# Kernel tuning notes

Measured on AMD Instinct MI355X. Metric: run time of the kernel, lower is better.

The kernel has to match this reference:

```python
import jax, jax.numpy as jnp
import numpy as np

B, T, D = 1, 8192, 1024
H, DH = 16, 64
WIN = 128          # attention window (tokens on each side)
WB = 128
NB = T // WB
EPS = 1e-5


def _layernorm(x, g, b):
    mu = jnp.mean(x, axis=-1, keepdims=True)
    var = jnp.mean(jnp.square(x - mu), axis=-1, keepdims=True)
    return (x - mu) * jax.lax.rsqrt(var + EPS) * g + b


def _band_mask():
    # query offset i in [0, WB), key offset j in [0, 3*WB) within [prev|self|next] blocks
    i = jnp.arange(WB)[:, None]
    j = jnp.arange(3 * WB)[None, :]
    rel = j - WB - i                      # key_pos - query_pos
    band = jnp.abs(rel) <= WIN            # sliding window |i-j| <= W (matches torch mask)
    blk = jnp.arange(NB)[:, None, None]
    key_pos = blk * WB + (j - WB)[None]   # absolute key position
    return band[None] & (key_pos >= 0) & (key_pos < T)   # [NB, WB, 3*WB]


def _local_attention(q, k, v):
    # q,k,v: [B,H,T,DH] -> block-local SDPA, mathematically identical to
    # full SDPA with the additive band mask in the torch code.
    def blocks(t):
        return t.reshape(B, H, NB, WB, DH)
    qb = blocks(q)
    kp = jnp.pad(blocks(k), ((0, 0), (0, 0), (1, 1), (0, 0), (0, 0)))
    vp = jnp.pad(blocks(v), ((0, 0), (0, 0), (1, 1), (0, 0), (0, 0)))
    # gather [prev, self, next] key/value blocks: [B,H,NB,3*WB,DH]
    k3 = jnp.concatenate([kp[:, :, s:s + NB] for s in range(3)], axis=3)
    v3 = jnp.concatenate([vp[:, :, s:s + NB] for s in range(3)], axis=3)
    scores = jnp.einsum('bhnqd,bhnkd->bhnqk', qb, k3) / np.sqrt(DH).astype(np.float32)
    mask = _band_mask()                                   # [NB,WB,3WB]
    scores = jnp.where(mask[None, None], scores, -jnp.inf)
    attn = jax.nn.softmax(scores, axis=-1)
    out = jnp.einsum('bhnqk,bhnkd->bhnqd', attn, v3)      # [B,H,NB,WB,DH]
    return out.reshape(B, H, T, DH)


def setup_inputs() -> dict:
    key = jax.random.key(0)
    ks = jax.random.split(key, 7)
    s = 0.02
    return {
        'x': jax.random.normal(ks[0], (B, T, D), jnp.float32),
        'wq': jax.random.normal(ks[1], (D, D), jnp.float32) * s,
        'wk': jax.random.normal(ks[2], (D, D), jnp.float32) * s,
        'wv': jax.random.normal(ks[3], (D, D), jnp.float32) * s,
        'wo': jax.random.normal(ks[4], (D, D), jnp.float32) * s,
        'wg': jax.random.normal(ks[5], (D, 2 * D), jnp.float32) * s,
        'wd': jax.random.normal(ks[6], (2 * D, D), jnp.float32) * s,
        'norm_g': jnp.ones((D,), jnp.float32),
        'norm_b': jnp.zeros((D,), jnp.float32),
        'ffn_g': jnp.ones((D,), jnp.float32),
        'ffn_b': jnp.zeros((D,), jnp.float32),
    }


def reference(x, wq, wk, wv, wo, wg, wd, norm_g, norm_b, ffn_g, ffn_b):
    h = _layernorm(x, norm_g, norm_b)
    def heads(t):  # [B,T,D] -> [B,H,T,DH]
        return t.reshape(B, T, H, DH).transpose(0, 2, 1, 3)
    q, k, v = heads(h @ wq), heads(h @ wk), heads(h @ wv)
    attn_out = _local_attention(q, k, v)                     # [B,H,T,DH]
    attn_out = attn_out.transpose(0, 2, 1, 3).reshape(B, T, D)
    x = x + attn_out @ wo
    h = _layernorm(x, ffn_g, ffn_b)
    x = x + jax.nn.silu(h @ wg) @ wd
    return x
```

## Files before the change

kernel.cpp:

```cpp
#include <hip/hip_runtime.h>
#include <cstdint>

#define T_DIM 8192
#define D_DIM 1024
#define NB_DIM 64
#define QKS 2048

typedef __bf16 bf16x8 __attribute__((ext_vector_type(8)));
typedef __bf16 bf16x4 __attribute__((ext_vector_type(4)));
typedef float f32x4 __attribute__((ext_vector_type(4)));

#define MFMA16(a, b, c) __builtin_amdgcn_mfma_f32_16x16x32_bf16((a), (b), (c), 0, 0, 0)
#define BAR() asm volatile("s_barrier" ::: "memory")
#define VMCNT(n) asm volatile("s_waitcnt vmcnt(" #n ")" ::: "memory")

__device__ __forceinline__ void gld_lds16(const void* gsrc, void* ldst) {
  __builtin_amdgcn_global_load_lds(
      (__attribute__((address_space(1))) void*)(uintptr_t)gsrc,
      (__attribute__((address_space(3))) void*)(uintptr_t)ldst,
      16, 0, 0);
}

__global__ __launch_bounds__(256) void transpose_all(
    const float* __restrict__ wq, const float* __restrict__ wk,
    const float* __restrict__ wv, const float* __restrict__ wo,
    const float* __restrict__ wg, const float* __restrict__ wd,
    __bf16* __restrict__ wqkT, __bf16* __restrict__ wvT,
    __bf16* __restrict__ woT, __bf16* __restrict__ wgT,
    __bf16* __restrict__ wdT) {
  __shared__ float tile[32][33];
  const int bid = (int)blockIdx.x;
  const float* W; __bf16* Wt; int K, N, n0, k0, local;
  if (bid < 1024)      { W = wq; Wt = wqkT;            K = 1024; N = 1024; local = bid; }
  else if (bid < 2048) { W = wk; Wt = wqkT + 1048576;  K = 1024; N = 1024; local = bid - 1024; }
  else if (bid < 3072) { W = wv; Wt = wvT;             K = 1024; N = 1024; local = bid - 2048; }
  else if (bid < 4096) { W = wo; Wt = woT;             K = 1024; N = 1024; local = bid - 3072; }
  else if (bid < 6144) { W = wg; Wt = wgT;             K = 1024; N = 2048; local = bid - 4096; }
  else                 { W = wd; Wt = wdT;             K = 2048; N = 1024; local = bid - 6144; }
  if (N == 2048) { n0 = (local & 63) * 32; k0 = (local >> 6) * 32; }
  else           { n0 = (local & 31) * 32; k0 = (local >> 5) * 32; }
  const int tx = threadIdx.x & 31, ty = threadIdx.x >> 5;
#pragma unroll
  for (int i = 0; i < 32; i += 8)
    tile[ty + i][tx] = W[(size_t)(k0 + ty + i) * N + n0 + tx];
  __syncthreads();
#pragma unroll
  for (int i = 0; i < 32; i += 8)
    Wt[(size_t)(n0 + ty + i) * K + k0 + tx] = (__bf16)tile[tx][ty + i];
}

template <typename TI>
__global__ __launch_bounds__(256) void ln_kernel(
    const TI* __restrict__ x, const float* __restrict__ g,
    const float* __restrict__ b, __bf16* __restrict__ out) {
  __shared__ float red[8];
  const int row = blockIdx.x, tid = threadIdx.x;
  float v0, v1, v2, v3;
  if constexpr (sizeof(TI) == 4) {
    const float4 v = ((const float4*)(x + (size_t)row * D_DIM))[tid];
    v0 = v.x; v1 = v.y; v2 = v.z; v3 = v.w;
  } else {
    const bf16x4 v = ((const bf16x4*)(x + (size_t)row * D_DIM))[tid];
    v0 = (float)v[0]; v1 = (float)v[1]; v2 = (float)v[2]; v3 = (float)v[3];
  }
  float s = v0 + v1 + v2 + v3;
#pragma unroll
  for (int off = 32; off >= 1; off >>= 1) s += __shfl_xor(s, off, 64);
  if ((tid & 63) == 0) red[tid >> 6] = s;
  __syncthreads();
  const float mean = (red[0] + red[1] + red[2] + red[3]) * (1.0f / D_DIM);
  const float d0 = v0 - mean, d1 = v1 - mean, d2 = v2 - mean, d3 = v3 - mean;
  float ss = d0 * d0 + d1 * d1 + d2 * d2 + d3 * d3;
#pragma unroll
  for (int off = 32; off >= 1; off >>= 1) ss += __shfl_xor(ss, off, 64);
  if ((tid & 63) == 0) red[4 + (tid >> 6)] = ss;
  __syncthreads();
  const float var = (red[4] + red[5] + red[6] + red[7]) * (1.0f / D_DIM);
  const float rstd = rsqrtf(var + 1e-5f);
  const float4 gg = ((const float4*)g)[tid];
  const float4 bb = ((const float4*)b)[tid];
  bf16x4 o;
  o[0] = (__bf16)(d0 * rstd * gg.x + bb.x);
  o[1] = (__bf16)(d1 * rstd * gg.y + bb.y);
  o[2] = (__bf16)(d2 * rstd * gg.z + bb.z);
  o[3] = (__bf16)(d3 * rstd * gg.w + bb.w);
  *(bf16x4*)(out + (size_t)row * D_DIM + tid * 4) = o;
}

template <int BM_, int EPI>
__global__ __launch_bounds__(512, 2) void gemm8(
    const __bf16* __restrict__ A, const __bf16* __restrict__ Bt,
    const void* __restrict__ Res, void* __restrict__ Cout,
    int M, int N, int K, int nbn) {
  constexpr int MF = BM_ / 32;
  constexpr int MH = MF / 2;
  constexpr int SA = 8 * MF;
  constexpr int LA = BM_ / 128;
  constexpr int ATILE = BM_ * 64;
  constexpr int AHALF = BM_ * 32;
  constexpr int BOFF = 2 * ATILE;
  __shared__ __bf16 lds[2 * BM_ * 64 + 32768];

  const int tid = threadIdx.x;
  const int l = tid & 63, w = tid >> 6;
  const int lr = l & 15, lg = l >> 4;
  const int wr = w >> 2, wc = w & 3;
  const int nwg = gridDim.x;
  const int bid = (int)blockIdx.x;
  const int swz = (bid & 7) * (nwg >> 3) + (bid >> 3);
  const int bm = swz / nbn, bn = swz % nbn;
  const int am0 = bm * BM_, bn0 = bn * 256;

  f32x4 acc[MF][4];
  const f32x4 z4 = {0.f, 0.f, 0.f, 0.f};
#pragma unroll
  for (int m = 0; m < MF; ++m)
#pragma unroll
    for (int n = 0; n < 4; ++n) acc[m][n] = z4;

  auto stageA = [&](int h, int b, int k0) {
#pragma unroll
    for (int r = 0; r < LA; ++r) {
      const int ci = r * 512 + tid;
      const int wri = ci >> 3, c8 = ci & 7;
      const int ra = (wri % SA) + (wri / SA) * (2 * SA) + h * SA;
      gld_lds16(A + (size_t)(am0 + ra) * K + k0 + ((c8 ^ (wri & 7)) << 3),
                (__bf16*)lds + b * ATILE + h * AHALF + ci * 8);
    }
  };
  auto stageB = [&](int h, int b, int k0) {
#pragma unroll
    for (int r = 0; r < 2; ++r) {
      const int ci = r * 512 + tid;
      const int wri = ci >> 3, c8 = ci & 7;
      const int rb = (wri & 31) + (wri >> 5) * 64 + h * 32;
      gld_lds16(Bt + (size_t)(bn0 + rb) * K + k0 + ((c8 ^ (wri & 7)) << 3),
                (__bf16*)lds + BOFF + b * 16384 + h * 8192 + ci * 8);
    }
  };

  const int x7 = lr & 7;
  const int aoff0 = (lr + wr * SA) * 64 + ((lg) ^ x7) * 8;
  const int aoff1 = (lr + wr * SA) * 64 + ((4 + lg) ^ x7) * 8;
  const int boff0 = BOFF + (lr + wc * 32) * 64 + ((lg) ^ x7) * 8;
  const int boff1 = BOFF + (lr + wc * 32) * 64 + ((4 + lg) ^ x7) * 8;

  const int nt = K >> 6;
  stageA(0, 0, 0);
  stageB(1, 0, 0);
  stageB(0, 0, 0);
  stageA(1, 0, 0);
  stageA(0, 1, 64);
  stageB(1, 1, 64);
  if constexpr (BM_ == 256) VMCNT(6); else VMCNT(4);
  BAR();

  int buf = 0;
  bf16x8 afr[MH][2], bfr0[2][2], bfr1[2][2];
  for (int t = 0; t < nt; ++t) {
    const bool s1 = (t + 1 < nt);
    const bool s2 = (t + 2 < nt);
    const int nb = buf ^ 1;
    const int k1 = (t + 1) << 6;
    const int k2 = (t + 2) << 6;
    const __bf16* pa0 = lds + buf * ATILE + aoff0;
    const __bf16* pa1 = lds + buf * ATILE + aoff1;
    const __bf16* pb0 = lds + buf * 16384 + boff0;
    const __bf16* pb1 = lds + buf * 16384 + boff1;

#pragma unroll
    for (int i = 0; i < MH; ++i) {
      afr[i][0] = *(const bf16x8*)(pa0 + i * 1024);
      afr[i][1] = *(const bf16x8*)(pa1 + i * 1024);
    }
#pragma unroll
    for (int j = 0; j < 2; ++j) {
      bfr0[j][0] = *(const bf16x8*)(pb0 + j * 1024);
      bfr0[j][1] = *(const bf16x8*)(pb1 + j * 1024);
    }
    if (s1) stageB(0, nb, k1);
    BAR();
    __builtin_amdgcn_s_setprio(1);
#pragma unroll
    for (int kk = 0; kk < 2; ++kk)
#pragma unroll
      for (int i = 0; i < MH; ++i)
#pragma unroll
        for (int j = 0; j < 2; ++j)
          acc[i][j] = MFMA16(afr[i][kk], bfr0[j][kk], acc[i][j]);
    __builtin_amdgcn_s_setprio(0);

#pragma unroll
    for (int j = 0; j < 2; ++j) {
      bfr1[j][0] = *(const bf16x8*)(pb0 + 8192 + j * 1024);
      bfr1[j][1] = *(const bf16x8*)(pb1 + 8192 + j * 1024);
    }
    if (s1) {
      stageA(1, nb, k1);
      if constexpr (BM_ == 256) VMCNT(8); else VMCNT(6);
    } else {
      VMCNT(0);
    }
    BAR();
    __builtin_amdgcn_s_setprio(1);
#pragma unroll
    for (int kk = 0; kk < 2; ++kk)
#pragma unroll
      for (int i = 0; i < MH; ++i)
#pragma unroll
        for (int j = 0; j < 2; ++j)
          acc[i][2 + j] = MFMA16(afr[i][kk], bfr1[j][kk], acc[i][2 + j]);
    __builtin_amdgcn_s_setprio(0);

#pragma unroll
    for (int i = 0; i < MH; ++i) {
      afr[i][0] = *(const bf16x8*)(pa0 + AHALF + i * 1024);
      afr[i][1] = *(const bf16x8*)(pa1 + AHALF + i * 1024);
    }
    if (s2) stageA(0, buf, k2);
    BAR();
    __builtin_amdgcn_s_setprio(1);
#pragma unroll
    for (int kk = 0; kk < 2; ++kk)
#pragma unroll
      for (int i = 0; i < MH; ++i)
#pragma unroll
        for (int j = 0; j < 2; ++j)
          acc[MH + i][2 + j] = MFMA16(afr[i][kk], bfr1[j][kk], acc[MH + i][2 + j]);
    __builtin_amdgcn_s_setprio(0);

    if (s2) {
      stageB(1, buf, k2);
      if constexpr (BM_ == 256) VMCNT(6); else VMCNT(4);
    } else if (s1) {
      if constexpr (BM_ == 256) VMCNT(2); else VMCNT(1);
    }
    BAR();
    __builtin_amdgcn_s_setprio(1);
#pragma unroll
    for (int kk = 0; kk < 2; ++kk)
#pragma unroll
      for (int i = 0; i < MH; ++i)
#pragma unroll
        for (int j = 0; j < 2; ++j)
          acc[MH + i][j] = MFMA16(afr[i][kk], bfr0[j][kk], acc[MH + i][j]);
    __builtin_amdgcn_s_setprio(0);

    buf = nb;
  }

  if constexpr (EPI == 5) {
    const __bf16* R = (const __bf16*)Res;
    float* O = (float*)Cout;
#pragma unroll
    for (int mf = 0; mf < MF; ++mf)
#pragma unroll
      for (int nf = 0; nf < 4; ++nf)
#pragma unroll
        for (int r = 0; r < 4; ++r) {
          const int row = am0 + wr * 2 * SA + mf * 16 + lg * 4 + r;
          const int col = bn0 + wc * 64 + nf * 16 + lr;
          const size_t idx = (size_t)row * N + col;
          O[idx] = acc[mf][nf][r] + (float)R[idx];
        }
  } else {
    __syncthreads();
    __bf16* Ct = (__bf16*)lds;
#pragma unroll
    for (int mf = 0; mf < MF; ++mf)
#pragma unroll
      for (int nf = 0; nf < 4; ++nf)
#pragma unroll
        for (int r = 0; r < 4; ++r) {
          const int rl = wr * 2 * SA + mf * 16 + lg * 4 + r;
          const int cl = wc * 64 + nf * 16 + lr;
          float v = acc[mf][nf][r];
          if constexpr (EPI == 3) v = v / (1.f + __expf(-v));
          if constexpr (EPI == 4)
            v += ((const float*)Res)[(size_t)(am0 + rl) * N + bn0 + cl];
          Ct[rl * 256 + (((cl >> 3) ^ (rl & 7)) << 3) + (cl & 7)] = (__bf16)v;
        }
    __syncthreads();
    __bf16* O = (__bf16*)Cout;
#pragma unroll
    for (int i = 0; i < BM_ / 16; ++i) {
      const int ci = i * 512 + tid;
      const int row = ci >> 5, c8 = ci & 31;
      *(bf16x8*)(O + (size_t)(am0 + row) * N + bn0 + c8 * 8) =
          *(const bf16x8*)&Ct[row * 256 + ((c8 ^ (row & 7)) << 3)];
    }
  }
}

__global__ __launch_bounds__(64, 2) void attn_kernel(
    const __bf16* __restrict__ qk, const __bf16* __restrict__ vT,
    __bf16* __restrict__ out) {
  __shared__ __bf16 Pw[32 * 136];

  const int l = (int)threadIdx.x;
  const int lr = l & 15, lg = l >> 4;
  const int bx = (int)blockIdx.x;
  const int swz = (bx & 7) * 512 + (bx >> 3);
  const int h = swz >> 8;
  const int blk = (swz >> 2) & 63;
  const int w = swz & 3;

  const __bf16* qbase =
      qk + (size_t)(blk * 128 + w * 32 + lr) * QKS + h * 64 + lg * 8;
  bf16x8 qf[2][2];
#pragma unroll
  for (int m = 0; m < 2; ++m)
#pragma unroll
    for (int ks = 0; ks < 2; ++ks)
      qf[m][ks] = *(const bf16x8*)(qbase + (size_t)m * 16 * QKS + ks * 32);

  const f32x4 z4 = {0.f, 0.f, 0.f, 0.f};
  float ssum[2][4];
  f32x4 o[2][4];
#pragma unroll
  for (int m = 0; m < 2; ++m) {
#pragma unroll
    for (int r = 0; r < 4; ++r) ssum[m][r] = 0.f;
#pragma unroll
    for (int n = 0; n < 4; ++n) o[m][n] = z4;
  }

  for (int it = 0; it < 3; ++it) {
    const int kb = blk + it - 1;
    if (kb < 0 || kb >= NB_DIM) continue;
    const int rel = it - 1;
    const int kclo = (rel < 0) ? (w * 2) : 0;
    const int kchi = (rel > 0) ? (w * 2 + 2) : 8;

    f32x4 s[2][8];
    const __bf16* kbase =
        qk + (size_t)(kb * 128 + lr) * QKS + 1024 + h * 64 + lg * 8;
#pragma unroll
    for (int kc = 0; kc < 8; ++kc) {
      if (kc < kclo || kc >= kchi) continue;
      const bf16x8 k0 = *(const bf16x8*)(kbase + (size_t)kc * 16 * QKS);
      const bf16x8 k1 = *(const bf16x8*)(kbase + (size_t)kc * 16 * QKS + 32);
      s[0][kc] = MFMA16(qf[0][0], k0, z4);
      s[1][kc] = MFMA16(qf[1][0], k0, z4);
      s[0][kc] = MFMA16(qf[0][1], k1, s[0][kc]);
      s[1][kc] = MFMA16(qf[1][1], k1, s[1][kc]);
    }

#pragma unroll
    for (int m = 0; m < 2; ++m) {
#pragma unroll
      for (int r = 0; r < 4; ++r) {
        const int qi = w * 32 + m * 16 + lg * 4 + r;
        float acc_s = 0.f;
#pragma unroll
        for (int kc = 0; kc < 8; ++kc) {
          if (kc < kclo || kc >= kchi) continue;
          const int kj = kc * 16 + lr;
          float p = __expf(s[m][kc][r] * 0.125f);
          const bool valid = (rel == 0) || (rel < 0 ? (kj >= qi) : (kj <= qi));
          p = valid ? p : 0.f;
          s[m][kc][r] = p;
          acc_s += p;
        }
        ssum[m][r] += acc_s;
      }
    }

#pragma unroll
    for (int m = 0; m < 2; ++m)
#pragma unroll
      for (int kc = 0; kc < 8; ++kc) {
        if (kc < kclo || kc >= kchi) continue;
#pragma unroll
        for (int r = 0; r < 4; ++r)
          Pw[(m * 16 + lg * 4 + r) * 136 + kc * 16 + lr] = (__bf16)s[m][kc][r];
      }

    const int kslo = kclo >> 1, kshi = kchi >> 1;
    const __bf16* vbase =
        vT + (size_t)(h * 64 + lr) * T_DIM + kb * 128 + lg * 8;
#pragma unroll
    for (int ks = 0; ks < 4; ++ks) {
      if (ks < kslo || ks >= kshi) continue;
      bf16x8 pa[2];
#pragma unroll
      for (int m = 0; m < 2; ++m)
        pa[m] = *(const bf16x8*)&Pw[(m * 16 + lr) * 136 + ks * 32 + lg * 8];
#pragma unroll
      for (int n = 0; n < 4; ++n) {
        const bf16x8 vb = *(const bf16x8*)(vbase + (size_t)n * 16 * T_DIM + ks * 32);
        o[0][n] = MFMA16(pa[0], vb, o[0][n]);
        o[1][n] = MFMA16(pa[1], vb, o[1][n]);
      }
    }
  }

  float inv[2][4];
#pragma unroll
  for (int m = 0; m < 2; ++m)
#pragma unroll
    for (int r = 0; r < 4; ++r) {
      float rs = ssum[m][r];
#pragma unroll
      for (int off = 1; off < 16; off <<= 1) rs += __shfl_xor(rs, off, 64);
      inv[m][r] = __builtin_amdgcn_rcpf(rs);
    }
#pragma unroll
  for (int m = 0; m < 2; ++m)
#pragma unroll
    for (int n = 0; n < 4; ++n)
#pragma unroll
      for (int r = 0; r < 4; ++r)
        Pw[(m * 16 + lg * 4 + r) * 136 + n * 16 + lr] =
            (__bf16)(o[m][n][r] * inv[m][r]);
#pragma unroll
  for (int i = 0; i < 4; ++i) {
    const int ci = i * 64 + l;
    const int qrow = ci >> 3;
    const int c8 = (ci & 7) * 8;
    const bf16x8 vv = *(const bf16x8*)&Pw[qrow * 136 + c8];
    *(bf16x8*)(out + (size_t)(blk * 128 + w * 32 + qrow) * D_DIM + h * 64 + c8) = vv;
  }
}

extern "C" void kernel_launch(void* const* d_in, const int* in_sizes, int n_in,
                              void* d_out, int out_size, void* d_ws, size_t ws_size,
                              hipStream_t stream) {
  (void)in_sizes; (void)n_in; (void)out_size; (void)ws_size;
  const float* x      = (const float*)d_in[0];
  const float* wq     = (const float*)d_in[1];
  const float* wk     = (const float*)d_in[2];
  const float* wv     = (const float*)d_in[3];
  const float* wo     = (const float*)d_in[4];
  const float* wg     = (const float*)d_in[5];
  const float* wd     = (const float*)d_in[6];
  const float* norm_g = (const float*)d_in[7];
  const float* norm_b = (const float*)d_in[8];
  const float* ffn_g  = (const float*)d_in[9];
  const float* ffn_b  = (const float*)d_in[10];
  float* out = (float*)d_out;

  char* ws = (char*)d_ws;
  constexpr size_t MB = 1ull << 20;
  __bf16* wqkT = (__bf16*)(ws + 0 * MB);
  __bf16* wvT  = (__bf16*)(ws + 4 * MB);
  __bf16* woT  = (__bf16*)(ws + 6 * MB);
  __bf16* wgT  = (__bf16*)(ws + 8 * MB);
  __bf16* wdT  = (__bf16*)(ws + 12 * MB);
  __bf16* hbuf = (__bf16*)(ws + 16 * MB);
  __bf16* qkbf = (__bf16*)(ws + 32 * MB);
  __bf16* gbf  = (__bf16*)(ws + 32 * MB);
  __bf16* vTbf = (__bf16*)(ws + 64 * MB);
  __bf16* x2bf = (__bf16*)(ws + 80 * MB);

  transpose_all<<<8192, 256, 0, stream>>>(wq, wk, wv, wo, wg, wd,
                                          wqkT, wvT, woT, wgT, wdT);

  ln_kernel<float><<<8192, 256, 0, stream>>>(x, norm_g, norm_b, hbuf);

  gemm8<256, 0><<<256, 512, 0, stream>>>(hbuf, wqkT, nullptr, qkbf,
                                         8192, 2048, 1024, 8);
  gemm8<128, 0><<<256, 512, 0, stream>>>(wvT, hbuf, nullptr, vTbf,
                                         1024, 8192, 1024, 32);

  attn_kernel<<<4096, 64, 0, stream>>>(qkbf, vTbf, hbuf);

  gemm8<128, 4><<<256, 512, 0, stream>>>(hbuf, woT, x, x2bf, 8192, 1024, 1024, 4);

  ln_kernel<__bf16><<<8192, 256, 0, stream>>>(x2bf, ffn_g, ffn_b, hbuf);

  gemm8<256, 3><<<256, 512, 0, stream>>>(hbuf, wgT, nullptr, gbf,
                                         8192, 2048, 1024, 8);

  gemm8<128, 5><<<256, 512, 0, stream>>>(gbf, wdT, x2bf, out, 8192, 1024, 2048, 4);
}
```

Measured before the change: 236.9 us.

## Merge weight transpose with first layernorm and batch QK and V GEMMs

The weight-transpose kernel and the first LayerNorm now run as one launch with 16384 blocks, split by block index. The QK projection (now tiled with BM=128, 512 tiles) and the transposed V projection (256 tiles) run as one dual-problem GEMM launch of 768 workgroups. Each sub-problem gets its own swizzle range. This removes two launches and the tail gaps between them, and fills the device better than two separate 256-block grids. The cost is that the QK GEMM moves from 256-row to 128-row tiles, which reduces reuse of the B operand.

```diff
diff --git a/kernel.cpp b/kernel.cpp
--- a/kernel.cpp
+++ b/kernel.cpp
@@ -21,48 +21,74 @@
       16, 0, 0);
 }
 
-__global__ __launch_bounds__(256) void transpose_all(
+__global__ __launch_bounds__(256) void prep_all(
     const float* __restrict__ wq, const float* __restrict__ wk,
     const float* __restrict__ wv, const float* __restrict__ wo,
     const float* __restrict__ wg, const float* __restrict__ wd,
     __bf16* __restrict__ wqkT, __bf16* __restrict__ wvT,
     __bf16* __restrict__ woT, __bf16* __restrict__ wgT,
-    __bf16* __restrict__ wdT) {
-  __shared__ float tile[32][33];
+    __bf16* __restrict__ wdT,
+    const float* __restrict__ x, const float* __restrict__ ng,
+    const float* __restrict__ nb, __bf16* __restrict__ h) {
+  __shared__ float smem_f[32 * 33];
   const int bid = (int)blockIdx.x;
-  const float* W; __bf16* Wt; int K, N, n0, k0, local;
-  if (bid < 1024)      { W = wq; Wt = wqkT;            K = 1024; N = 1024; local = bid; }
-  else if (bid < 2048) { W = wk; Wt = wqkT + 1048576;  K = 1024; N = 1024; local = bid - 1024; }
-  else if (bid < 3072) { W = wv; Wt = wvT;             K = 1024; N = 1024; local = bid - 2048; }
-  else if (bid < 4096) { W = wo; Wt = woT;             K = 1024; N = 1024; local = bid - 3072; }
-  else if (bid < 6144) { W = wg; Wt = wgT;             K = 1024; N = 2048; local = bid - 4096; }
-  else                 { W = wd; Wt = wdT;             K = 2048; N = 1024; local = bid - 6144; }
-  if (N == 2048) { n0 = (local & 63) * 32; k0 = (local >> 6) * 32; }
-  else           { n0 = (local & 31) * 32; k0 = (local >> 5) * 32; }
-  const int tx = threadIdx.x & 31, ty = threadIdx.x >> 5;
-#pragma unroll
-  for (int i = 0; i < 32; i += 8)
-    tile[ty + i][tx] = W[(size_t)(k0 + ty + i) * N + n0 + tx];
-  __syncthreads();
-#pragma unroll
-  for (int i = 0; i < 32; i += 8)
-    Wt[(size_t)(n0 + ty + i) * K + k0 + tx] = (__bf16)tile[tx][ty + i];
+  const int tid = threadIdx.x;
+
+  if (bid < 8192) {
+    float (*tile)[33] = (float(*)[33])smem_f;
+    const float* W; __bf16* Wt; int K, N, n0, k0, local;
+    if (bid < 1024)      { W = wq; Wt = wqkT;            K = 1024; N = 1024; local = bid; }
+    else if (bid < 2048) { W = wk; Wt = wqkT + 1048576;  K = 1024; N = 1024; local = bid - 1024; }
+    else if (bid < 3072) { W = wv; Wt = wvT;             K = 1024; N = 1024; local = bid - 2048; }
+    else if (bid < 4096) { W = wo; Wt = woT;             K = 1024; N = 1024; local = bid - 3072; }
+    else if (bid < 6144) { W = wg; Wt = wgT;             K = 1024; N = 2048; local = bid - 4096; }
+    else                 { W = wd; Wt = wdT;             K = 2048; N = 1024; local = bid - 6144; }
+    if (N == 2048) { n0 = (local & 63) * 32; k0 = (local >> 6) * 32; }
+    else           { n0 = (local & 31) * 32; k0 = (local >> 5) * 32; }
+    const int tx = tid & 31, ty = tid >> 5;
+#pragma unroll
+    for (int i = 0; i < 32; i += 8)
+      tile[ty + i][tx] = W[(size_t)(k0 + ty + i) * N + n0 + tx];
+    __syncthreads();
+#pragma unroll
+    for (int i = 0; i < 32; i += 8)
+      Wt[(size_t)(n0 + ty + i) * K + k0 + tx] = (__bf16)tile[tx][ty + i];
+  } else {
+    float* red = smem_f;
+    const int row = bid - 8192;
+    const float4 v = ((const float4*)(x + (size_t)row * D_DIM))[tid];
+    float s = v.x + v.y + v.z + v.w;
+#pragma unroll
+    for (int off = 32; off >= 1; off >>= 1) s += __shfl_xor(s, off, 64);
+    if ((tid & 63) == 0) red[tid >> 6] = s;
+    __syncthreads();
+    const float mean = (red[0] + red[1] + red[2] + red[3]) * (1.0f / D_DIM);
+    const float d0 = v.x - mean, d1 = v.y - mean, d2 = v.z - mean, d3 = v.w - mean;
+    float ss = d0 * d0 + d1 * d1 + d2 * d2 + d3 * d3;
+#pragma unroll
+    for (int off = 32; off >= 1; off >>= 1) ss += __shfl_xor(ss, off, 64);
+    if ((tid & 63) == 0) red[4 + (tid >> 6)] = ss;
+    __syncthreads();
+    const float var = (red[4] + red[5] + red[6] + red[7]) * (1.0f / D_DIM);
+    const float rstd = rsqrtf(var + 1e-5f);
+    const float4 gg = ((const float4*)ng)[tid];
+    const float4 bb = ((const float4*)nb)[tid];
+    bf16x4 o;
+    o[0] = (__bf16)(d0 * rstd * gg.x + bb.x);
+    o[1] = (__bf16)(d1 * rstd * gg.y + bb.y);
+    o[2] = (__bf16)(d2 * rstd * gg.z + bb.z);
+    o[3] = (__bf16)(d3 * rstd * gg.w + bb.w);
+    *(bf16x4*)(h + (size_t)row * D_DIM + tid * 4) = o;
+  }
 }
 
-template <typename TI>
 __global__ __launch_bounds__(256) void ln_kernel(
-    const TI* __restrict__ x, const float* __restrict__ g,
+    const __bf16* __restrict__ x, const float* __restrict__ g,
     const float* __restrict__ b, __bf16* __restrict__ out) {
   __shared__ float red[8];
   const int row = blockIdx.x, tid = threadIdx.x;
-  float v0, v1, v2, v3;
-  if constexpr (sizeof(TI) == 4) {
-    const float4 v = ((const float4*)(x + (size_t)row * D_DIM))[tid];
-    v0 = v.x; v1 = v.y; v2 = v.z; v3 = v.w;
-  } else {
-    const bf16x4 v = ((const bf16x4*)(x + (size_t)row * D_DIM))[tid];
-    v0 = (float)v[0]; v1 = (float)v[1]; v2 = (float)v[2]; v3 = (float)v[3];
-  }
+  const bf16x4 v = ((const bf16x4*)(x + (size_t)row * D_DIM))[tid];
+  const float v0 = (float)v[0], v1 = (float)v[1], v2 = (float)v[2], v3 = (float)v[3];
   float s = v0 + v1 + v2 + v3;
 #pragma unroll
   for (int off = 32; off >= 1; off >>= 1) s += __shfl_xor(s, off, 64);
@@ -87,11 +113,12 @@
   *(bf16x4*)(out + (size_t)row * D_DIM + tid * 4) = o;
 }
 
-template <int BM_, int EPI>
+template <int BM_, int EPI, bool DUAL>
 __global__ __launch_bounds__(512, 2) void gemm8(
-    const __bf16* __restrict__ A, const __bf16* __restrict__ Bt,
-    const void* __restrict__ Res, void* __restrict__ Cout,
-    int M, int N, int K, int nbn) {
+    const __bf16* Ap, const __bf16* Btp, const void* Res, void* Coutp,
+    int Mp, int Np, int K, int nbnp, int split,
+    const __bf16* A2, const __bf16* Bt2, void* Cout2,
+    int M2, int N2, int nbn2) {
   constexpr int MF = BM_ / 32;
   constexpr int MH = MF / 2;
   constexpr int SA = 8 * MF;
@@ -101,12 +128,26 @@
   constexpr int BOFF = 2 * ATILE;
   __shared__ __bf16 lds[2 * BM_ * 64 + 32768];
 
+  const __bf16* A = Ap;
+  const __bf16* Bt = Btp;
+  void* Cout = Coutp;
+  int M = Mp, N = Np, nbn = nbnp;
+  int bid = (int)blockIdx.x;
+  int nwg = gridDim.x;
+  if constexpr (DUAL) {
+    if (bid >= split) {
+      A = A2; Bt = Bt2; Cout = Cout2; M = M2; N = N2; nbn = nbn2;
+      bid -= split; nwg = gridDim.x - split;
+    } else {
+      nwg = split;
+    }
+  }
+  (void)M;
+
   const int tid = threadIdx.x;
   const int l = tid & 63, w = tid >> 6;
   const int lr = l & 15, lg = l >> 4;
   const int wr = w >> 2, wc = w & 3;
-  const int nwg = gridDim.x;
-  const int bid = (int)blockIdx.x;
   const int swz = (bid & 7) * (nwg >> 3) + (bid >> 3);
   const int bm = swz / nbn, bn = swz % nbn;
   const int am0 = bm * BM_, bn0 = bn * 256;
@@ -160,7 +201,7 @@
   for (int t = 0; t < nt; ++t) {
     const bool s1 = (t + 1 < nt);
     const bool s2 = (t + 2 < nt);
-    const int nb = buf ^ 1;
+    const int nb_ = buf ^ 1;
     const int k1 = (t + 1) << 6;
     const int k2 = (t + 2) << 6;
     const __bf16* pa0 = lds + buf * ATILE + aoff0;
@@ -178,7 +219,7 @@
       bfr0[j][0] = *(const bf16x8*)(pb0 + j * 1024);
       bfr0[j][1] = *(const bf16x8*)(pb1 + j * 1024);
     }
-    if (s1) stageB(0, nb, k1);
+    if (s1) stageB(0, nb_, k1);
     BAR();
     __builtin_amdgcn_s_setprio(1);
 #pragma unroll
@@ -196,7 +237,7 @@
       bfr1[j][1] = *(const bf16x8*)(pb1 + 8192 + j * 1024);
     }
     if (s1) {
-      stageA(1, nb, k1);
+      stageA(1, nb_, k1);
       if constexpr (BM_ == 256) VMCNT(8); else VMCNT(6);
     } else {
       VMCNT(0);
@@ -246,7 +287,7 @@
           acc[MH + i][j] = MFMA16(afr[i][kk], bfr0[j][kk], acc[MH + i][j]);
     __builtin_amdgcn_s_setprio(0);
 
-    buf = nb;
+    buf = nb_;
   }
 
   if constexpr (EPI == 5) {
@@ -453,24 +494,27 @@
   __bf16* vTbf = (__bf16*)(ws + 64 * MB);
   __bf16* x2bf = (__bf16*)(ws + 80 * MB);
 
-  transpose_all<<<8192, 256, 0, stream>>>(wq, wk, wv, wo, wg, wd,
-                                          wqkT, wvT, woT, wgT, wdT);
-
-  ln_kernel<float><<<8192, 256, 0, stream>>>(x, norm_g, norm_b, hbuf);
-
-  gemm8<256, 0><<<256, 512, 0, stream>>>(hbuf, wqkT, nullptr, qkbf,
-                                         8192, 2048, 1024, 8);
-  gemm8<128, 0><<<256, 512, 0, stream>>>(wvT, hbuf, nullptr, vTbf,
-                                         1024, 8192, 1024, 32);
+  prep_all<<<16384, 256, 0, stream>>>(wq, wk, wv, wo, wg, wd,
+                                      wqkT, wvT, woT, wgT, wdT,
+                                      x, norm_g, norm_b, hbuf);
+
+  gemm8<128, 0, true><<<768, 512, 0, stream>>>(
+      hbuf, wqkT, nullptr, qkbf, 8192, 2048, 1024, 8, 512,
+      wvT, hbuf, vTbf, 1024, 8192, 32);
 
   attn_kernel<<<4096, 64, 0, stream>>>(qkbf, vTbf, hbuf);
 
-  gemm8<128, 4><<<256, 512, 0, stream>>>(hbuf, woT, x, x2bf, 8192, 1024, 1024, 4);
-
-  ln_kernel<__bf16><<<8192, 256, 0, stream>>>(x2bf, ffn_g, ffn_b, hbuf);
-
-  gemm8<256, 3><<<256, 512, 0, stream>>>(hbuf, wgT, nullptr, gbf,
-                                         8192, 2048, 1024, 8);
-
-  gemm8<128, 5><<<256, 512, 0, stream>>>(gbf, wdT, x2bf, out, 8192, 1024, 2048, 4);
+  gemm8<128, 4, false><<<256, 512, 0, stream>>>(
+      hbuf, woT, x, x2bf, 8192, 1024, 1024, 4, 0,
+      nullptr, nullptr, nullptr, 0, 0, 1);
+
+  ln_kernel<<<8192, 256, 0, stream>>>(x2bf, ffn_g, ffn_b, hbuf);
+
+  gemm8<256, 3, false><<<256, 512, 0, stream>>>(
+      hbuf, wgT, nullptr, gbf, 8192, 2048, 1024, 8, 0,
+      nullptr, nullptr, nullptr, 0, 0, 1);
+
+  gemm8<128, 5, false><<<256, 512, 0, stream>>>(
+      gbf, wdT, x2bf, out, 8192, 1024, 2048, 4, 0,
+      nullptr, nullptr, nullptr, 0, 0, 1);
 }
```

Result: no change. 237.4 us (+0.2%).
